# Kernel tuning notes

Measured on AMD Instinct MI355X. Metric: run time of the kernel, lower is better.

Reference implementation:

```python
import jax, jax.numpy as jnp
import numpy as np

B, D, C, N = 256, 512, 345, 50000
K = 5
ALPHA = 1.0
EPS = 1e-12


def setup_inputs() -> dict:
    key = jax.random.key(0)
    k1, k2, k3, k4, k5 = jax.random.split(key, 5)
    return {
        "features": jax.random.normal(k1, (B, D), dtype=jnp.float32),
        "predictions": jax.random.normal(k2, (B, C), dtype=jnp.float32),
        "fea_bank": jax.random.normal(k3, (N, D), dtype=jnp.float32),
        "score_bank": jax.random.uniform(k4, (N, C), dtype=jnp.float32, minval=1e-3, maxval=1.0),
        "trg_idx": jax.random.randint(k5, (B,), 0, N, dtype=jnp.int64),
    }


def reference(features, predictions, fea_bank, score_bank, trg_idx):
    softmax_out = jax.nn.softmax(predictions, axis=1)  # [B, C]

    # --- no_grad block: bank update + neighbor retrieval ---
    f_norm = features / jnp.maximum(
        jnp.linalg.norm(features, axis=1, keepdims=True), EPS
    )
    f_ng = jax.lax.stop_gradient(f_norm)
    s_ng = jax.lax.stop_gradient(softmax_out)
    fb = fea_bank.at[trg_idx].set(f_ng)       # [N, D]
    sb = score_bank.at[trg_idx].set(s_ng)     # [N, C]
    distance = f_ng @ fb.T                    # [B, N] cosine similarity
    _, idx_near = jax.lax.top_k(distance, K + 1)
    idx_near = idx_near[:, 1:]                # drop self -> [B, K]
    score_near = sb[idx_near]                 # [B, K, C]

    # F.kl_div(input=softmax_out (NOT log), target=score_near):
    # target * (log(target) - input), summed over C and K, mean over B.
    kl = score_near * (jnp.log(score_near) - softmax_out[:, None, :])
    loss = jnp.mean(kl.sum(-1).sum(-1))

    # dispersion: masked pairwise dot of softmax outputs (off-diagonal)
    dot = softmax_out @ softmax_out.T         # [B, B]
    mask = 1.0 - jnp.eye(B, dtype=dot.dtype)
    neg_pred = jnp.mean((dot * mask).sum(-1))
    loss = loss + ALPHA * neg_pred
    return loss
```

## Files before the change

### kernel.cpp

```cpp
#include <hip/hip_runtime.h>
#include <cstdint>

#define BB 256
#define DD 512
#define CC 345
#define NBANK 50000
#define NPAD 50048
#define KNEI 5
#define ALPHAC 1.0f
#define EPSN 1e-12f
#define NTILES 391
#define NHALF (NTILES * 2)
#define CSLOTS (NTILES * 4)

typedef short short8 __attribute__((ext_vector_type(8)));
typedef float f32x4 __attribute__((ext_vector_type(4)));
typedef unsigned long long u64;

__device__ inline uint32_t f2bf1(float x) {
    union { float f; uint32_t u; } v; v.f = x;
    return (v.u + 0x7FFFu + ((v.u >> 16) & 1u)) >> 16;
}
__device__ inline uint32_t pack2(float a, float b) {
    return f2bf1(a) | (f2bf1(b) << 16);
}
__device__ inline float bl(uint32_t x) {
    union { uint32_t u; float f; } v; v.u = x << 16; return v.f;
}
__device__ inline float bh(uint32_t x) {
    union { uint32_t u; float f; } v; v.u = x & 0xFFFF0000u; return v.f;
}
__device__ inline u64 mkkey(float v, int j) {
    union { float f; uint32_t u; } c; c.f = v;
    uint32_t b = c.u;
    uint32_t k = (b & 0x80000000u) ? ~b : (b | 0x80000000u);
    return ((u64)k << 32) | (uint32_t)(~j);
}
__device__ inline u64 umax64(u64 a, u64 b) { return a > b ? a : b; }
__device__ inline u64 shfl_xor_u64(u64 v, int m) {
    int lo = __shfl_xor((int)(uint32_t)v, m, 64);
    int hi = __shfl_xor((int)(v >> 32), m, 64);
    return ((u64)(uint32_t)hi << 32) | (uint32_t)lo;
}
__device__ inline void ins6u(u64 k, u64* lv) {
    if (k > lv[5]) {
        int q = 5;
        while (q > 0 && k > lv[q - 1]) { lv[q] = lv[q - 1]; q--; }
        lv[q] = k;
    }
}
__device__ inline void tree6u(u64* sv, int t, const u64* lv) {
#pragma unroll
    for (int r = 0; r < 6; r++) sv[t * 6 + r] = lv[r];
    __syncthreads();
    for (int s = 128; s > 0; s >>= 1) {
        if (t < s) {
            u64 av[6], bv[6], rv[6];
#pragma unroll
            for (int r = 0; r < 6; r++) { av[r] = sv[t * 6 + r]; bv[r] = sv[(t + s) * 6 + r]; }
            int x = 0, y = 0;
#pragma unroll
            for (int o = 0; o < 6; o++) {
                bool pk = av[x] > bv[y];
                rv[o] = pk ? av[x] : bv[y];
                x += pk; y += !pk;
            }
#pragma unroll
            for (int r = 0; r < 6; r++) sv[t * 6 + r] = rv[r];
        }
        __syncthreads();
    }
}
__device__ inline void async16(const void* g, void* l) {
    __builtin_amdgcn_global_load_lds(
        (const __attribute__((address_space(1))) unsigned int*)g,
        (__attribute__((address_space(3))) unsigned int*)l, 16, 0, 0);
}
__device__ inline size_t sw_off(int tile, int r, int ch) {
    return (size_t)tile * 8192 + r * 64 + ((ch ^ (r & 7)) * 8);
}

__global__ void winner_kernel(const int* __restrict__ trg, int* __restrict__ win,
                              float* __restrict__ out) {
    int t = threadIdx.x;
    __shared__ int st[BB];
    if (t == 0) out[0] = 0.f;
    st[t] = trg[t];
    __syncthreads();
    int mv = st[t];
    int w = 1;
    for (int b2 = t + 1; b2 < BB; b2++)
        if (st[b2] == mv) w = 0;
    win[t] = w;
}

__global__ void norm_softmax_kernel(const float* __restrict__ feat,
                                    const float* __restrict__ pred,
                                    unsigned short* __restrict__ fnb,
                                    unsigned short* __restrict__ fnb2,
                                    float* __restrict__ p) {
    int b = blockIdx.x, t = threadIdx.x;
    __shared__ float red[256];
    float x0 = feat[b * DD + t];
    float x1 = feat[b * DD + t + 256];
    red[t] = x0 * x0 + x1 * x1;
    __syncthreads();
    for (int s = 128; s > 0; s >>= 1) {
        if (t < s) red[t] += red[t + s];
        __syncthreads();
    }
    float inv = 1.0f / fmaxf(sqrtf(red[0]), EPSN);
    if (t < 64) {
        const f32x4* src = (const f32x4*)(feat + b * DD + t * 8);
        f32x4 f0 = src[0], f1 = src[1];
        uint4 u = make_uint4(pack2(f0[0] * inv, f0[1] * inv),
                             pack2(f0[2] * inv, f0[3] * inv),
                             pack2(f1[0] * inv, f1[1] * inv),
                             pack2(f1[2] * inv, f1[3] * inv));
        *(uint4*)(fnb + b * DD + t * 8) = u;
        int mtile = b >> 7, r = b & 127, kt = t >> 3, ch = t & 7;
        *(uint4*)(fnb2 + sw_off(mtile * 8 + kt, r, ch)) = u;
    }
    __syncthreads();
    float y0 = (t < CC) ? pred[b * CC + t] : -3.0e38f;
    float y1 = (t + 256 < CC) ? pred[b * CC + t + 256] : -3.0e38f;
    red[t] = fmaxf(y0, y1);
    __syncthreads();
    for (int s = 128; s > 0; s >>= 1) {
        if (t < s) red[t] = fmaxf(red[t], red[t + s]);
        __syncthreads();
    }
    float M = red[0];
    __syncthreads();
    float e0 = (t < CC) ? expf(y0 - M) : 0.f;
    float e1 = (t + 256 < CC) ? expf(y1 - M) : 0.f;
    red[t] = e0 + e1;
    __syncthreads();
    for (int s = 128; s > 0; s >>= 1) {
        if (t < s) red[t] += red[t + s];
        __syncthreads();
    }
    float si = 1.0f / red[0];
    if (t < CC) p[b * CC + t] = e0 * si;
    if (t + 256 < CC) p[b * CC + t + 256] = e1 * si;
}

__global__ void convert_kernel(const float* __restrict__ bank,
                               unsigned short* __restrict__ bankb) {
    int tid = blockIdx.x * 256 + threadIdx.x;
    int j = tid >> 6, c = tid & 63;
    int kt = c >> 3, ch = c & 7;
    int r = j & 127, nt = j >> 7;
    uint4 val = make_uint4(0, 0, 0, 0);
    if (j < NBANK) {
        const f32x4* s = (const f32x4*)(bank + (size_t)j * DD + kt * 64 + ch * 8);
        f32x4 f0 = s[0], f1 = s[1];
        val = make_uint4(pack2(f0[0], f0[1]), pack2(f0[2], f0[3]),
                         pack2(f1[0], f1[1]), pack2(f1[2], f1[3]));
    }
    *(uint4*)(bankb + sw_off(nt * 8 + kt, r, ch)) = val;
}

__global__ void patch_kernel(const unsigned short* __restrict__ fnb,
                             const int* __restrict__ trg, const int* __restrict__ win,
                             unsigned short* __restrict__ bankb) {
    int b = blockIdx.x;
    if (!win[b]) return;
    int t = threadIdx.x;
    int j = trg[b];
    int nt = j >> 7, r = j & 127, kt = t >> 3, ch = t & 7;
    uint4 v = *(const uint4*)(fnb + b * DD + t * 8);
    *(uint4*)(bankb + sw_off(nt * 8 + kt, r, ch)) = v;
}

__global__ __launch_bounds__(256) void gemm_topk_kernel(
        const unsigned short* __restrict__ fnb2, const unsigned short* __restrict__ bankb,
        u64* __restrict__ cand) {
    __shared__ __align__(16) char smem[32768];
    unsigned short* As = (unsigned short*)smem;
    unsigned short* Bs = (unsigned short*)(smem + 16384);

    int t = threadIdx.x;
    int ntb = blockIdx.x >> 1, mtile = blockIdx.x & 1;
    int w = t >> 6, lane = t & 63, quad = lane >> 4, l16 = lane & 15;
    int wm = w >> 1, wn = w & 1;
    int j0 = ntb * 128;

    f32x4 acc[4][4];
#pragma unroll
    for (int mt = 0; mt < 4; mt++)
#pragma unroll
        for (int nt = 0; nt < 4; nt++)
            acc[mt][nt] = (f32x4){0.f, 0.f, 0.f, 0.f};

    const char* Ag = (const char*)fnb2 + (size_t)mtile * 8 * 16384;
    const char* Bg = (const char*)bankb + (size_t)ntb * 8 * 16384;

    for (int kt = 0; kt < 8; kt++) {
        size_t tb = (size_t)kt * 16384;
        int co = w * 4096 + lane * 16;
#pragma unroll
        for (int u = 0; u < 4; u++)
            async16(Ag + tb + co + u * 1024, smem + w * 4096 + u * 1024);
#pragma unroll
        for (int u = 0; u < 4; u++)
            async16(Bg + tb + co + u * 1024, smem + 16384 + w * 4096 + u * 1024);
        __syncthreads();
#pragma unroll
        for (int ks = 0; ks < 2; ks++) {
            int sw = ((ks * 4 + quad) ^ (l16 & 7)) * 8;
            short8 af[4], bf[4];
#pragma unroll
            for (int mt = 0; mt < 4; mt++)
                af[mt] = *(const short8*)(As + (wm * 64 + mt * 16 + l16) * 64 + sw);
#pragma unroll
            for (int nt = 0; nt < 4; nt++)
                bf[nt] = *(const short8*)(Bs + (wn * 64 + nt * 16 + l16) * 64 + sw);
#pragma unroll
            for (int mt = 0; mt < 4; mt++)
#pragma unroll
                for (int nt = 0; nt < 4; nt++)
                    acc[mt][nt] = __builtin_amdgcn_mfma_f32_16x16x32_bf16(
                        af[mt], bf[nt], acc[mt][nt], 0, 0, 0);
        }
        __syncthreads();
    }

    bool maskPad[4];
#pragma unroll
    for (int nt = 0; nt < 4; nt++)
        maskPad[nt] = (ntb == NTILES - 1) && ((j0 + wn * 64 + nt * 16 + l16) >= NBANK);

#pragma unroll
    for (int mt = 0; mt < 4; mt++)
#pragma unroll
        for (int r2 = 0; r2 < 4; r2++) {
            u64 k[4];
#pragma unroll
            for (int nt = 0; nt < 4; nt++) {
                int j = j0 + wn * 64 + nt * 16 + l16;
                k[nt] = maskPad[nt] ? 0ull : mkkey(acc[mt][nt][r2], j);
            }
            u64 m = umax64(umax64(k[0], k[1]), umax64(k[2], k[3]));
#pragma unroll
            for (int off = 1; off < 16; off <<= 1)
                m = umax64(m, shfl_xor_u64(m, off));
            u64 top1 = m;
#pragma unroll
            for (int nt = 0; nt < 4; nt++) k[nt] = (k[nt] == top1) ? 0ull : k[nt];
            m = umax64(umax64(k[0], k[1]), umax64(k[2], k[3]));
#pragma unroll
            for (int off = 1; off < 16; off <<= 1)
                m = umax64(m, shfl_xor_u64(m, off));
            if (l16 == 0) {
                int gi = mtile * 128 + wm * 64 + mt * 16 + quad * 4 + r2;
                u64* cp = cand + (size_t)gi * CSLOTS + (ntb * 2 + wn) * 2;
                cp[0] = top1; cp[1] = m;
            }
        }
}

__global__ __launch_bounds__(256) void merge_kernel(
        const u64* __restrict__ cand, const unsigned short* __restrict__ fnb,
        const unsigned short* __restrict__ bankb, int* __restrict__ nidx) {
    int i = blockIdx.x, t = threadIdx.x;
    __shared__ u64 sv[1536];
    __shared__ uint32_t fm[25];
    __shared__ int fl[128];
    __shared__ int nf;
    __shared__ float a[512];
    const u64* cr = cand + (size_t)i * CSLOTS;

    u64 lv[6] = {0, 0, 0, 0, 0, 0};
    for (int q = t; q < CSLOTS; q += 256) ins6u(cr[q], lv);
    if (t < 25) fm[t] = 0;
    if (t == 0) nf = 0;
    tree6u(sv, t, lv);
    u64 M6 = sv[5];
    __syncthreads();
    for (int h = t; h < NHALF; h += 256) {
        if (cr[h * 2 + 1] >= M6) {
            int s = atomicAdd(&nf, 1);
            if (s < 128) fl[s] = h;
            atomicOr(&fm[h >> 5], 1u << (h & 31));
        }
    }
    __syncthreads();
    if (nf > 0) {
        uint32_t wrd = ((const uint32_t*)(fnb + (size_t)i * DD))[t];
        a[2 * t] = bl(wrd);
        a[2 * t + 1] = bh(wrd);
        __syncthreads();
        u64 l2[6] = {0, 0, 0, 0, 0, 0};
        for (int q = t; q < CSLOTS; q += 256) {
            int h = q >> 1;
            if (!((fm[h >> 5] >> (h & 31)) & 1u)) ins6u(cr[q], l2);
        }
        int nfl = nf < 128 ? nf : 128;
        for (int s = 0; s < nfl; s++) {
            int h = fl[s];
            if (t < 64) {
                int nt2 = h >> 1;
                int r = (h & 1) * 64 + t;
                int j = nt2 * 128 + r;
                if (j < NBANK) {
                    int rx = r & 7;
                    float dot = 0.f;
                    for (int kt = 0; kt < 8; kt++) {
                        const uint4* q4 = (const uint4*)(bankb + (size_t)(nt2 * 8 + kt) * 8192 + r * 64);
                        const float* ab = a + kt * 64;
#pragma unroll
                        for (int pp = 0; pp < 8; pp++) {
                            uint4 u = q4[pp];
                            const float* av = ab + ((pp ^ rx) << 3);
                            dot += bl(u.x) * av[0] + bh(u.x) * av[1]
                                 + bl(u.y) * av[2] + bh(u.y) * av[3]
                                 + bl(u.z) * av[4] + bh(u.z) * av[5]
                                 + bl(u.w) * av[6] + bh(u.w) * av[7];
                        }
                    }
                    ins6u(mkkey(dot, j), l2);
                }
            }
        }
        __syncthreads();
        tree6u(sv, t, l2);
    }
    if (t == 0) {
#pragma unroll
        for (int r = 1; r < 6; r++)
            nidx[i * KNEI + r - 1] = (int)(~(uint32_t)(sv[r] & 0xFFFFFFFFull));
    }
}

__global__ void kl_negpred_kernel(const float* __restrict__ p,
                                  const float* __restrict__ sbank,
                                  const int* __restrict__ nidx,
                                  const int* __restrict__ trg,
                                  float* __restrict__ out) {
    int bid = blockIdx.x, t = threadIdx.x;
    __shared__ float red[256];
    __shared__ float aux[256];
    if (bid < BB) {
        int b = bid;
        __shared__ int st[BB];
        __shared__ int sj[KNEI], sb[KNEI];
        st[t] = trg[t];
        __syncthreads();
        if (t < KNEI) {
            int j = nidx[b * KNEI + t];
            sj[t] = j;
            int src = -1;
            for (int b2 = 0; b2 < BB; b2++)
                if (st[b2] == j) src = b2;
            sb[t] = src;
        }
        __syncthreads();
        float local = 0.f;
        for (int k = 0; k < KNEI; k++) {
            int j = sj[k], src = sb[k];
            const float* srow = (src >= 0) ? (p + src * CC) : (sbank + (size_t)j * CC);
            for (int c = t; c < CC; c += 256) {
                float s = srow[c];
                local += s * (logf(s) - p[b * CC + c]);
            }
        }
        red[t] = local;
        __syncthreads();
        for (int s = 128; s > 0; s >>= 1) {
            if (t < s) red[t] += red[t + s];
            __syncthreads();
        }
        if (t == 0) atomicAdd(out, red[0] * (1.0f / BB));
    } else {
        int c = bid - BB;
        float v = p[t * CC + c];
        red[t] = v;
        aux[t] = v * v;
        __syncthreads();
        for (int s = 128; s > 0; s >>= 1) {
            if (t < s) { red[t] += red[t + s]; aux[t] += aux[t + s]; }
            __syncthreads();
        }
        if (t == 0) atomicAdd(out, ALPHAC * (red[0] * red[0] - aux[0]) * (1.0f / BB));
    }
}

extern "C" void kernel_launch(void* const* d_in, const int* in_sizes, int n_in,
                              void* d_out, int out_size, void* d_ws, size_t ws_size,
                              hipStream_t stream) {
    const float* feat  = (const float*)d_in[0];
    const float* pred  = (const float*)d_in[1];
    const float* bank  = (const float*)d_in[2];
    const float* sbank = (const float*)d_in[3];
    const int*   trg   = (const int*)d_in[4];
    float* out = (float*)d_out;

    char* ws = (char*)d_ws;
    unsigned short* fnb2  = (unsigned short*)ws;
    unsigned short* fnb   = (unsigned short*)(ws + 262144);
    unsigned short* bankb = (unsigned short*)(ws + 524288);
    float*          p     = (float*)(ws + 51773440);
    int*            win   = (int*)(ws + 52126720);
    u64*            cand  = (u64*)(ws + 52127744);
    int*            nidx  = (int*)(ws + 55330816);

    winner_kernel<<<1, 256, 0, stream>>>(trg, win, out);
    norm_softmax_kernel<<<BB, 256, 0, stream>>>(feat, pred, fnb, fnb2, p);
    convert_kernel<<<(NPAD * 64) / 256, 256, 0, stream>>>(bank, bankb);
    patch_kernel<<<BB, 64, 0, stream>>>(fnb, trg, win, bankb);
    gemm_topk_kernel<<<NTILES * 2, 256, 0, stream>>>(fnb2, bankb, cand);
    merge_kernel<<<BB, 256, 0, stream>>>(cand, fnb, bankb, nidx);
    kl_negpred_kernel<<<BB + CC, 256, 0, stream>>>(p, sbank, nidx, trg, out);
}
```

Measured before the change: 284.3 us.

## Fuse bank bf16 conversion and scatter patch into GEMM tile loads

Drops the separate convert and patch kernels that wrote a full swizzled bf16 copy of the 50000x512 bank. The GEMM now reads fp32 bank rows directly, converts them to bf16 in registers and writes them into LDS. Overwritten rows come from a replacement index map built by new init and winner kernels. The tile shape changes so each block covers 64 bank rows against all 256 queries, which removes the duplicate B-tile reads. The cost is synchronous global loads plus conversion inside the GEMM main loop and a slower scalar fp32 path in the merge recompute.

```diff
diff --git a/kernel.cpp b/kernel.cpp
--- a/kernel.cpp
+++ b/kernel.cpp
@@ -9,9 +9,8 @@
 #define KNEI 5
 #define ALPHAC 1.0f
 #define EPSN 1e-12f
-#define NTILES 391
-#define NHALF (NTILES * 2)
-#define CSLOTS (NTILES * 4)
+#define NHALF 782
+#define CSLOTS (NHALF * 2)
 
 typedef short short8 __attribute__((ext_vector_type(8)));
 typedef float f32x4 __attribute__((ext_vector_type(4)));
@@ -80,7 +79,12 @@
     return (size_t)tile * 8192 + r * 64 + ((ch ^ (r & 7)) * 8);
 }
 
-__global__ void winner_kernel(const int* __restrict__ trg, int* __restrict__ win,
+__global__ void repl_init_kernel(int* __restrict__ repl) {
+    int idx = blockIdx.x * 256 + threadIdx.x;
+    if (idx < NPAD) repl[idx] = -1;
+}
+
+__global__ void winner_kernel(const int* __restrict__ trg, int* __restrict__ repl,
                               float* __restrict__ out) {
     int t = threadIdx.x;
     __shared__ int st[BB];
@@ -91,7 +95,7 @@
     int w = 1;
     for (int b2 = t + 1; b2 < BB; b2++)
         if (st[b2] == mv) w = 0;
-    win[t] = w;
+    if (w) repl[mv] = t;
 }
 
 __global__ void norm_softmax_kernel(const float* __restrict__ feat,
@@ -145,46 +149,22 @@
     if (t + 256 < CC) p[b * CC + t + 256] = e1 * si;
 }
 
-__global__ void convert_kernel(const float* __restrict__ bank,
-                               unsigned short* __restrict__ bankb) {
-    int tid = blockIdx.x * 256 + threadIdx.x;
-    int j = tid >> 6, c = tid & 63;
-    int kt = c >> 3, ch = c & 7;
-    int r = j & 127, nt = j >> 7;
-    uint4 val = make_uint4(0, 0, 0, 0);
-    if (j < NBANK) {
-        const f32x4* s = (const f32x4*)(bank + (size_t)j * DD + kt * 64 + ch * 8);
-        f32x4 f0 = s[0], f1 = s[1];
-        val = make_uint4(pack2(f0[0], f0[1]), pack2(f0[2], f0[3]),
-                         pack2(f1[0], f1[1]), pack2(f1[2], f1[3]));
-    }
-    *(uint4*)(bankb + sw_off(nt * 8 + kt, r, ch)) = val;
-}
-
-__global__ void patch_kernel(const unsigned short* __restrict__ fnb,
-                             const int* __restrict__ trg, const int* __restrict__ win,
-                             unsigned short* __restrict__ bankb) {
-    int b = blockIdx.x;
-    if (!win[b]) return;
+__global__ __launch_bounds__(256) void gemm_topk_kernel(
+        const unsigned short* __restrict__ fnb2, const float* __restrict__ bank,
+        const unsigned short* __restrict__ fnb, const int* __restrict__ repl,
+        u64* __restrict__ cand) {
+    __shared__ __align__(16) char smem[40960];
+    unsigned short* As = (unsigned short*)smem;
+    unsigned short* Bs = (unsigned short*)(smem + 32768);
+
     int t = threadIdx.x;
-    int j = trg[b];
-    int nt = j >> 7, r = j & 127, kt = t >> 3, ch = t & 7;
-    uint4 v = *(const uint4*)(fnb + b * DD + t * 8);
-    *(uint4*)(bankb + sw_off(nt * 8 + kt, r, ch)) = v;
-}
-
-__global__ __launch_bounds__(256) void gemm_topk_kernel(
-        const unsigned short* __restrict__ fnb2, const unsigned short* __restrict__ bankb,
-        u64* __restrict__ cand) {
-    __shared__ __align__(16) char smem[32768];
-    unsigned short* As = (unsigned short*)smem;
-    unsigned short* Bs = (unsigned short*)(smem + 16384);
-
-    int t = threadIdx.x;
-    int ntb = blockIdx.x >> 1, mtile = blockIdx.x & 1;
+    int ntb = blockIdx.x;
+    int j0 = ntb * 64;
     int w = t >> 6, lane = t & 63, quad = lane >> 4, l16 = lane & 15;
-    int wm = w >> 1, wn = w & 1;
-    int j0 = ntb * 128;
+
+    int br = t >> 2, cq = t & 3;
+    int bj = j0 + br;
+    int rp = (bj < NBANK) ? repl[bj] : -2;
 
     f32x4 acc[4][4];
 #pragma unroll
@@ -193,29 +173,45 @@
         for (int nt = 0; nt < 4; nt++)
             acc[mt][nt] = (f32x4){0.f, 0.f, 0.f, 0.f};
 
-    const char* Ag = (const char*)fnb2 + (size_t)mtile * 8 * 16384;
-    const char* Bg = (const char*)bankb + (size_t)ntb * 8 * 16384;
+    const char* fnb2b = (const char*)fnb2;
 
     for (int kt = 0; kt < 8; kt++) {
-        size_t tb = (size_t)kt * 16384;
-        int co = w * 4096 + lane * 16;
-#pragma unroll
-        for (int u = 0; u < 4; u++)
-            async16(Ag + tb + co + u * 1024, smem + w * 4096 + u * 1024);
-#pragma unroll
-        for (int u = 0; u < 4; u++)
-            async16(Bg + tb + co + u * 1024, smem + 16384 + w * 4096 + u * 1024);
+        const char* asrc = fnb2b + (size_t)((w < 2 ? kt : kt + 8) * 16384 + (w & 1) * 8192);
+        char* adst = smem + w * 8192;
+#pragma unroll
+        for (int u = 0; u < 8; u++)
+            async16(asrc + u * 1024 + lane * 16, adst + u * 1024);
+        {
+            uint4 b0, b1;
+            if (rp >= 0) {
+                const uint4* s = (const uint4*)(fnb + (size_t)rp * DD + kt * 64 + cq * 16);
+                b0 = s[0]; b1 = s[1];
+            } else if (rp == -1) {
+                const f32x4* s = (const f32x4*)(bank + (size_t)bj * DD + kt * 64 + cq * 16);
+                f32x4 f0 = s[0], f1 = s[1], f2 = s[2], f3 = s[3];
+                b0 = make_uint4(pack2(f0[0], f0[1]), pack2(f0[2], f0[3]),
+                                pack2(f1[0], f1[1]), pack2(f1[2], f1[3]));
+                b1 = make_uint4(pack2(f2[0], f2[1]), pack2(f2[2], f2[3]),
+                                pack2(f3[0], f3[1]), pack2(f3[2], f3[3]));
+            } else {
+                b0 = make_uint4(0, 0, 0, 0);
+                b1 = make_uint4(0, 0, 0, 0);
+            }
+            int c0 = cq * 2;
+            *(uint4*)(Bs + br * 64 + ((c0 ^ (br & 7)) * 8)) = b0;
+            *(uint4*)(Bs + br * 64 + (((c0 + 1) ^ (br & 7)) * 8)) = b1;
+        }
         __syncthreads();
 #pragma unroll
         for (int ks = 0; ks < 2; ks++) {
-            int sw = ((ks * 4 + quad) ^ (l16 & 7)) * 8;
+            int swz = ((ks * 4 + quad) ^ (l16 & 7)) * 8;
             short8 af[4], bf[4];
 #pragma unroll
             for (int mt = 0; mt < 4; mt++)
-                af[mt] = *(const short8*)(As + (wm * 64 + mt * 16 + l16) * 64 + sw);
+                af[mt] = *(const short8*)(As + (w * 64 + mt * 16 + l16) * 64 + swz);
 #pragma unroll
             for (int nt = 0; nt < 4; nt++)
-                bf[nt] = *(const short8*)(Bs + (wn * 64 + nt * 16 + l16) * 64 + sw);
+                bf[nt] = *(const short8*)(Bs + (nt * 16 + l16) * 64 + swz);
 #pragma unroll
             for (int mt = 0; mt < 4; mt++)
 #pragma unroll
@@ -229,7 +225,7 @@
     bool maskPad[4];
 #pragma unroll
     for (int nt = 0; nt < 4; nt++)
-        maskPad[nt] = (ntb == NTILES - 1) && ((j0 + wn * 64 + nt * 16 + l16) >= NBANK);
+        maskPad[nt] = (ntb == NHALF - 1) && ((j0 + nt * 16 + l16) >= NBANK);
 
 #pragma unroll
     for (int mt = 0; mt < 4; mt++)
@@ -238,7 +234,7 @@
             u64 k[4];
 #pragma unroll
             for (int nt = 0; nt < 4; nt++) {
-                int j = j0 + wn * 64 + nt * 16 + l16;
+                int j = j0 + nt * 16 + l16;
                 k[nt] = maskPad[nt] ? 0ull : mkkey(acc[mt][nt][r2], j);
             }
             u64 m = umax64(umax64(k[0], k[1]), umax64(k[2], k[3]));
@@ -253,8 +249,8 @@
             for (int off = 1; off < 16; off <<= 1)
                 m = umax64(m, shfl_xor_u64(m, off));
             if (l16 == 0) {
-                int gi = mtile * 128 + wm * 64 + mt * 16 + quad * 4 + r2;
-                u64* cp = cand + (size_t)gi * CSLOTS + (ntb * 2 + wn) * 2;
+                int gi = w * 64 + mt * 16 + quad * 4 + r2;
+                u64* cp = cand + (size_t)gi * CSLOTS + ntb * 2;
                 cp[0] = top1; cp[1] = m;
             }
         }
@@ -262,7 +258,8 @@
 
 __global__ __launch_bounds__(256) void merge_kernel(
         const u64* __restrict__ cand, const unsigned short* __restrict__ fnb,
-        const unsigned short* __restrict__ bankb, int* __restrict__ nidx) {
+        const float* __restrict__ bank, const int* __restrict__ repl,
+        int* __restrict__ nidx) {
     int i = blockIdx.x, t = threadIdx.x;
     __shared__ u64 sv[1536];
     __shared__ uint32_t fm[25];
@@ -300,24 +297,20 @@
         for (int s = 0; s < nfl; s++) {
             int h = fl[s];
             if (t < 64) {
-                int nt2 = h >> 1;
-                int r = (h & 1) * 64 + t;
-                int j = nt2 * 128 + r;
+                int j = h * 64 + t;
                 if (j < NBANK) {
-                    int rx = r & 7;
+                    int rp = repl[j];
                     float dot = 0.f;
-                    for (int kt = 0; kt < 8; kt++) {
-                        const uint4* q4 = (const uint4*)(bankb + (size_t)(nt2 * 8 + kt) * 8192 + r * 64);
-                        const float* ab = a + kt * 64;
-#pragma unroll
-                        for (int pp = 0; pp < 8; pp++) {
-                            uint4 u = q4[pp];
-                            const float* av = ab + ((pp ^ rx) << 3);
-                            dot += bl(u.x) * av[0] + bh(u.x) * av[1]
-                                 + bl(u.y) * av[2] + bh(u.y) * av[3]
-                                 + bl(u.z) * av[4] + bh(u.z) * av[5]
-                                 + bl(u.w) * av[6] + bh(u.w) * av[7];
+                    if (rp >= 0) {
+                        const uint32_t* rw = (const uint32_t*)(fnb + (size_t)rp * DD);
+                        for (int kk = 0; kk < 256; kk++) {
+                            uint32_t u = rw[kk];
+                            dot += bl(u) * a[2 * kk] + bh(u) * a[2 * kk + 1];
                         }
+                    } else {
+                        const float* rw = bank + (size_t)j * DD;
+                        for (int kk = 0; kk < DD; kk++)
+                            dot += bl(f2bf1(rw[kk])) * a[kk];
                     }
                     ins6u(mkkey(dot, j), l2);
                 }
@@ -397,19 +390,17 @@
     float* out = (float*)d_out;
 
     char* ws = (char*)d_ws;
-    unsigned short* fnb2  = (unsigned short*)ws;
-    unsigned short* fnb   = (unsigned short*)(ws + 262144);
-    unsigned short* bankb = (unsigned short*)(ws + 524288);
-    float*          p     = (float*)(ws + 51773440);
-    int*            win   = (int*)(ws + 52126720);
-    u64*            cand  = (u64*)(ws + 52127744);
-    int*            nidx  = (int*)(ws + 55330816);
-
-    winner_kernel<<<1, 256, 0, stream>>>(trg, win, out);
+    unsigned short* fnb2 = (unsigned short*)ws;
+    unsigned short* fnb  = (unsigned short*)(ws + 262144);
+    float*          p    = (float*)(ws + 524288);
+    int*            repl = (int*)(ws + 877568);
+    u64*            cand = (u64*)(ws + 1077760);
+    int*            nidx = (int*)(ws + 4280832);
+
+    repl_init_kernel<<<(NPAD + 255) / 256, 256, 0, stream>>>(repl);
+    winner_kernel<<<1, 256, 0, stream>>>(trg, repl, out);
     norm_softmax_kernel<<<BB, 256, 0, stream>>>(feat, pred, fnb, fnb2, p);
-    convert_kernel<<<(NPAD * 64) / 256, 256, 0, stream>>>(bank, bankb);
-    patch_kernel<<<BB, 64, 0, stream>>>(fnb, trg, win, bankb);
-    gemm_topk_kernel<<<NTILES * 2, 256, 0, stream>>>(fnb2, bankb, cand);
-    merge_kernel<<<BB, 256, 0, stream>>>(cand, fnb, bankb, nidx);
+    gemm_topk_kernel<<<NHALF, 256, 0, stream>>>(fnb2, bank, fnb, repl, cand);
+    merge_kernel<<<BB, 256, 0, stream>>>(cand, fnb, bank, repl, nidx);
     kl_negpred_kernel<<<BB + CC, 256, 0, stream>>>(p, sbank, nidx, trg, out);
 }
```

Result: faster. 272.3 us (-4.2%).
